# Kernel optimization log

Measured on AMD Instinct MI355X. Metric: run time of the kernel, lower is better.

Reference implementation:

```python
import jax, jax.numpy as jnp
import numpy as np

N = 50000      # nodes
E = 800000     # edges (before self loops)
IN = 61        # input node features
H = 256        # hidden
HEADS = 8
C = H // HEADS # per-head channels = 32
L = 4          # GAT layers
EPS = 1e-5


def setup_inputs() -> dict:
    key = jax.random.key(0)
    ks = jax.random.split(key, 10)
    s = 0.05
    return {
        "x": jax.random.normal(ks[0], (N, IN), jnp.float32),
        "edge_index": jax.random.randint(ks[1], (2, E), 0, N),
        "in_W": jax.random.normal(ks[2], (IN, H), jnp.float32) * s,
        "in_b": jnp.zeros((H,), jnp.float32),
        "in_gamma": jnp.ones((H,), jnp.float32),
        "in_beta": jnp.zeros((H,), jnp.float32),
        "Ws": jax.random.normal(ks[3], (L, H, H), jnp.float32) * s,
        "att_src": jax.random.normal(ks[4], (L, HEADS, C), jnp.float32) * s,
        "att_dst": jax.random.normal(ks[5], (L, HEADS, C), jnp.float32) * s,
        "conv_b": jnp.zeros((L, H), jnp.float32),
        "bn_gamma": jnp.ones((L, H), jnp.float32),
        "bn_beta": jnp.zeros((L, H), jnp.float32),
        "mean_W": jax.random.normal(ks[6], (H, 1), jnp.float32) * s,
        "mean_b": jnp.zeros((1,), jnp.float32),
        "lv_W": jax.random.normal(ks[7], (H, 1), jnp.float32) * s,
        "lv_b": jnp.zeros((1,), jnp.float32),
    }


def _bn(h, gamma, beta):
    # training-mode BatchNorm1d: batch stats, biased variance
    mu = h.mean(axis=0)
    var = jnp.var(h, axis=0)
    return (h - mu) * jax.lax.rsqrt(var + EPS) * gamma + beta


def _gat_layer(h, src, dst, W, a_src, a_dst, bias):
    # h: [N,H] -> z: [N,HEADS,C]
    z = (h @ W).reshape(N, HEADS, C)
    e_src = jnp.einsum('nhc,hc->nh', z, a_src)  # [N,HEADS]
    e_dst = jnp.einsum('nhc,hc->nh', z, a_dst)
    e = jax.nn.leaky_relu(e_src[src] + e_dst[dst], 0.2)  # [Etot,HEADS]
    # segment softmax over destination neighborhoods
    emax = jax.ops.segment_max(e, dst, num_segments=N)
    p = jnp.exp(e - emax[dst])
    denom = jax.ops.segment_sum(p, dst, num_segments=N)
    alpha = p / denom[dst]
    # weighted scatter-aggregate of per-edge messages
    out = jax.ops.segment_sum(z[src] * alpha[:, :, None], dst, num_segments=N)
    return out.reshape(N, H) + bias


def reference(x, edge_index, in_W, in_b, in_gamma, in_beta, Ws, att_src,
              att_dst, conv_b, bn_gamma, bn_beta, mean_W, mean_b, lv_W, lv_b):
    loops = jnp.arange(N, dtype=edge_index.dtype)
    src = jnp.concatenate([edge_index[0], loops])  # add_self_loops=True
    dst = jnp.concatenate([edge_index[1], loops])
    # input projection: Linear -> BN -> ReLU (dropout off, deterministic)
    h = jax.nn.relu(_bn(x @ in_W + in_b, in_gamma, in_beta))
    for i in range(L):
        res = h
        h = _gat_layer(h, src, dst, Ws[i], att_src[i], att_dst[i], conv_b[i])
        h = jax.nn.relu(_bn(h, bn_gamma[i], bn_beta[i])) + res
    mean = (h @ mean_W + mean_b)[:, 0]
    log_var = jnp.clip((h @ lv_W + lv_b)[:, 0], -10.0, 10.0)
    return (mean, log_var)
```

## Files before the change

### kernel.cpp

```cpp
#include <hip/hip_runtime.h>
#include <hip/hip_fp16.h>

#define NN 50000
#define EE 800000
#define ETOT 850000
#define KIN 61
#define HH 256
#define NH 8
#define CC 32
#define LL 4
#define SCAN_NBLK 49

typedef __attribute__((ext_vector_type(8))) short bf16x8;
typedef __attribute__((ext_vector_type(4))) float f32x4;

__device__ __forceinline__ unsigned short f2b(float f) {
    unsigned u = __builtin_bit_cast(unsigned, f);
    u += 0x7fffu + ((u >> 16) & 1u);
    return (unsigned short)(u >> 16);
}
__device__ __forceinline__ float b2f(unsigned short h) {
    unsigned u = ((unsigned)h) << 16;
    return __builtin_bit_cast(float, u);
}
__device__ __forceinline__ unsigned short f2h(float f) {
    __half h = __float2half(f);
    return __builtin_bit_cast(unsigned short, h);
}

__device__ __forceinline__ void gload16(const void* g, void* l) {
    __builtin_amdgcn_global_load_lds(
        (const __attribute__((address_space(1))) void*)g,
        (__attribute__((address_space(3))) void*)l, 16, 0, 0);
}


__global__ __launch_bounds__(256) void edge_hist(const int* __restrict__ ei,
                                                 int* __restrict__ counts) {
    int e = blockIdx.x * 256 + threadIdx.x;
    if (e >= ETOT) return;
    int d = (e < EE) ? ei[EE + e] : (e - EE);
    atomicAdd(&counts[d], 1);
}

__global__ __launch_bounds__(256) void scan1(const int* __restrict__ counts,
                                             int* __restrict__ tmp,
                                             int* __restrict__ bsums) {
    __shared__ int lds[256];
    int b = blockIdx.x, t = threadIdx.x;
    int base = b * 1024 + t * 4;
    int v0 = 0, v1 = 0, v2 = 0, v3 = 0;
    if (base + 0 < NN) v0 = counts[base + 0];
    if (base + 1 < NN) v1 = counts[base + 1];
    if (base + 2 < NN) v2 = counts[base + 2];
    if (base + 3 < NN) v3 = counts[base + 3];
    int s = v0 + v1 + v2 + v3;
    lds[t] = s;
    __syncthreads();
    for (int off = 1; off < 256; off <<= 1) {
        int x = (t >= off) ? lds[t - off] : 0;
        __syncthreads();
        lds[t] += x;
        __syncthreads();
    }
    int run = lds[t] - s;
    if (t == 255) bsums[b] = lds[255];
    run += v0; if (base + 0 < NN) tmp[base + 0] = run;
    run += v1; if (base + 1 < NN) tmp[base + 1] = run;
    run += v2; if (base + 2 < NN) tmp[base + 2] = run;
    run += v3; if (base + 3 < NN) tmp[base + 3] = run;
}

__global__ void scan2(int* __restrict__ bsums) {
    if (threadIdx.x == 0) {
        int acc = 0;
        for (int i = 0; i < SCAN_NBLK; ++i) { int t = bsums[i]; bsums[i] = acc; acc += t; }
    }
}

__global__ __launch_bounds__(256) void scan3(const int* __restrict__ tmp,
                                             const int* __restrict__ bsums,
                                             const int* __restrict__ counts,
                                             int* __restrict__ rowptr,
                                             int* __restrict__ cursor) {
    int i = blockIdx.x * 256 + threadIdx.x;
    if (i >= NN) return;
    int incl = tmp[i] + bsums[i >> 10];
    rowptr[i + 1] = incl;
    cursor[i] = incl - counts[i];
    if (i == 0) rowptr[0] = 0;
}

__global__ __launch_bounds__(256) void edge_scatter(const int* __restrict__ ei,
                                                    int* __restrict__ cursor,
                                                    int* __restrict__ ssrc) {
    int e = blockIdx.x * 256 + threadIdx.x;
    if (e >= ETOT) return;
    int s, d;
    if (e < EE) { s = ei[e]; d = ei[EE + e]; } else { s = d = e - EE; }
    int pos = atomicAdd(&cursor[d], 1);
    ssrc[pos] = s;
}

__global__ __launch_bounds__(256) void sort_rows(const int* __restrict__ rowptr,
                                                 int* __restrict__ ssrc) {
    int wid = (blockIdx.x * 256 + threadIdx.x) >> 6;
    int lane = threadIdx.x & 63;
    if (wid >= NN) return;
    int beg = rowptr[wid], end = rowptr[wid + 1];
    int L = end - beg;
    if (L > 64) return;
    int v = (lane < L) ? ssrc[beg + lane] : 0x7fffffff;
#pragma unroll
    for (int k = 2; k <= 64; k <<= 1) {
#pragma unroll
        for (int j = k >> 1; j > 0; j >>= 1) {
            int partner = __shfl_xor(v, j);
            bool up = ((lane & k) == 0);
            bool keepMin = (up == ((lane & j) == 0));
            int mn = min(v, partner), mx = max(v, partner);
            v = keepMin ? mn : mx;
        }
    }
    if (lane < L) ssrc[beg + lane] = v;
}


__global__ __launch_bounds__(256) void prep_wt(const float* __restrict__ Ws,
                                               unsigned short* __restrict__ WT) {
    int t = blockIdx.x * 256 + threadIdx.x;
    if (t >= LL * HH * HH) return;
    int l = t >> 16, rem = t & 65535;
    int n = rem >> 8, k = rem & 255;
    WT[t] = f2b(Ws[l * 65536 + k * HH + n]);
}

__global__ __launch_bounds__(256) void prep_inwt(const float* __restrict__ in_W,
                                                 unsigned short* __restrict__ WT) {
    int t = blockIdx.x * 256 + threadIdx.x;
    if (t >= HH * 64) return;
    int n = t >> 6, k = t & 63;
    WT[t] = (k < KIN) ? f2b(in_W[k * HH + n]) : 0;
}

__global__ __launch_bounds__(256) void prep_x(const float* __restrict__ x,
                                              unsigned short* __restrict__ xb) {
    int t = blockIdx.x * 256 + threadIdx.x;
    if (t >= NN * 64) return;
    int n = t >> 6, c = t & 63;
    xb[t] = (c < KIN) ? f2b(x[n * KIN + c]) : 0;
}

template<int MODE>
__global__ __launch_bounds__(512) void gemm_mfma(const unsigned short* __restrict__ Asrc,
                                                 const unsigned short* __restrict__ Bt,
                                                 unsigned short* __restrict__ C,
                                                 const float* __restrict__ asl,
                                                 const float* __restrict__ adl,
                                                 float* __restrict__ esrcT,
                                                 float* __restrict__ edstT,
                                                 const float* __restrict__ sums,
                                                 const float* __restrict__ gamma,
                                                 const float* __restrict__ beta,
                                                 const unsigned short* __restrict__ res,
                                                 unsigned short* __restrict__ hbNew,
                                                 int M, int K) {
    __shared__ unsigned short As[128 * 64];
    __shared__ unsigned short Bs[256 * 64];
    __shared__ float scaleS[256], shiftS[256];
    int row0 = blockIdx.x * 128;
    int tid = threadIdx.x;
    int w = tid >> 6, l = tid & 63;
    int wm = w >> 2, wn = w & 3;
    int r15 = l & 15, q = l >> 4;

    if constexpr (MODE == 1) {
        if (tid < 256) {
            const float invN = 1.f / NN;
            float mn = sums[tid] * invN;
            float var = fmaxf(sums[256 + tid] * invN - mn * mn, 0.f);
            float rs = rsqrtf(var + 1e-5f);
            float sc = rs * gamma[tid];
            scaleS[tid] = sc;
            shiftS[tid] = beta[tid] - mn * sc;
        }
        __syncthreads();
    }

    f32x4 acc[4][4] = {};

    int crow = l >> 3;
    int cs   = l & 7;

    for (int kt = 0; kt < K; kt += 64) {
        if (kt) __syncthreads();
#pragma unroll
        for (int c = 0; c < 2; ++c) {
            int r = w * 16 + c * 8 + crow;
            int sg = cs ^ (r & 7);
            int ga = row0 + r;
            if constexpr (MODE == 0) {
                if (ga >= M) ga = M - 1;
                gload16(&Asrc[(size_t)ga * K + kt + sg * 8], &As[(w * 16 + c * 8) * 64]);
            } else {
                unsigned short* dst = &As[(w * 16 + c * 8) * 64 + l * 8];
                if (ga < M) {
                    int ch = kt + sg * 8;
                    ushort4 xlo = *(const ushort4*)&Asrc[(size_t)ga * 256 + ch];
                    ushort4 xhi = *(const ushort4*)&Asrc[(size_t)ga * 256 + ch + 4];
                    float4 sc0 = *(const float4*)&scaleS[ch];
                    float4 sc1 = *(const float4*)&scaleS[ch + 4];
                    float4 sh0 = *(const float4*)&shiftS[ch];
                    float4 sh1 = *(const float4*)&shiftS[ch + 4];
                    float f0 = fmaxf(b2f(xlo.x) * sc0.x + sh0.x, 0.f);
                    float f1 = fmaxf(b2f(xlo.y) * sc0.y + sh0.y, 0.f);
                    float f2 = fmaxf(b2f(xlo.z) * sc0.z + sh0.z, 0.f);
                    float f3 = fmaxf(b2f(xlo.w) * sc0.w + sh0.w, 0.f);
                    float f4 = fmaxf(b2f(xhi.x) * sc1.x + sh1.x, 0.f);
                    float f5 = fmaxf(b2f(xhi.y) * sc1.y + sh1.y, 0.f);
                    float f6 = fmaxf(b2f(xhi.z) * sc1.z + sh1.z, 0.f);
                    float f7 = fmaxf(b2f(xhi.w) * sc1.w + sh1.w, 0.f);
                    if (res) {
                        ushort4 rlo = *(const ushort4*)&res[(size_t)ga * 256 + ch];
                        ushort4 rhi = *(const ushort4*)&res[(size_t)ga * 256 + ch + 4];
                        f0 += b2f(rlo.x); f1 += b2f(rlo.y); f2 += b2f(rlo.z); f3 += b2f(rlo.w);
                        f4 += b2f(rhi.x); f5 += b2f(rhi.y); f6 += b2f(rhi.z); f7 += b2f(rhi.w);
                    }
                    ushort4 olo, ohi;
                    olo.x = f2b(f0); olo.y = f2b(f1); olo.z = f2b(f2); olo.w = f2b(f3);
                    ohi.x = f2b(f4); ohi.y = f2b(f5); ohi.z = f2b(f6); ohi.w = f2b(f7);
                    *(ushort4*)dst = olo;
                    *(ushort4*)(dst + 4) = ohi;
                    *(ushort4*)&hbNew[(size_t)ga * 256 + ch] = olo;
                    *(ushort4*)&hbNew[(size_t)ga * 256 + ch + 4] = ohi;
                } else {
                    ushort4 zz = {0, 0, 0, 0};
                    *(ushort4*)dst = zz;
                    *(ushort4*)(dst + 4) = zz;
                }
            }
        }
#pragma unroll
        for (int c = 0; c < 4; ++c) {
            int r = w * 32 + c * 8 + crow;
            int sg = cs ^ (r & 7);
            gload16(&Bt[(size_t)r * K + kt + sg * 8], &Bs[(w * 32 + c * 8) * 64]);
        }
        __syncthreads();
#pragma unroll
        for (int kk = 0; kk < 2; ++kk) {
            bf16x8 aF[4], bF[4];
#pragma unroll
            for (int i = 0; i < 4; ++i) {
                int ar = wm * 64 + i * 16 + r15;
                aF[i] = *(bf16x8*)&As[ar * 64 + ((kk * 4 + q) ^ (ar & 7)) * 8];
                int br = wn * 64 + i * 16 + r15;
                bF[i] = *(bf16x8*)&Bs[br * 64 + ((kk * 4 + q) ^ (br & 7)) * 8];
            }
#pragma unroll
            for (int i = 0; i < 4; ++i)
#pragma unroll
                for (int j = 0; j < 4; ++j)
                    acc[i][j] = __builtin_amdgcn_mfma_f32_16x16x32_bf16(aF[i], bF[j], acc[i][j], 0, 0, 0);
        }
    }

#pragma unroll
    for (int i = 0; i < 4; ++i)
#pragma unroll
        for (int j = 0; j < 4; ++j) {
            int nc = wn * 64 + j * 16 + r15;
#pragma unroll
            for (int r = 0; r < 4; ++r) {
                int gr = row0 + wm * 64 + i * 16 + q * 4 + r;
                if (gr < M) {
                    if (MODE == 1)
                        C[(size_t)(nc >> 5) * NN * CC + (size_t)gr * CC + (nc & 31)] = f2h(acc[i][j][r]);
                    else
                        C[(size_t)gr * HH + nc] = f2b(acc[i][j][r]);
                }
            }
        }

    if constexpr (MODE == 1) {
        int hdbase = wn * 2;
        float as_[4], ad_[4];
#pragma unroll
        for (int j = 0; j < 4; ++j) {
            int idx = (hdbase + (j >> 1)) * CC + (j & 1) * 16 + r15;
            as_[j] = asl[idx];
            ad_[j] = adl[idx];
        }
#pragma unroll
        for (int h = 0; h < 2; ++h) {
#pragma unroll
            for (int i = 0; i < 4; ++i) {
                float pes[4], ped[4];
#pragma unroll
                for (int r = 0; r < 4; ++r) {
                    float v0 = __half2float(__float2half(acc[i][2 * h][r]));
                    float v1 = __half2float(__float2half(acc[i][2 * h + 1][r]));
                    pes[r] = v0 * as_[2 * h] + v1 * as_[2 * h + 1];
                    ped[r] = v0 * ad_[2 * h] + v1 * ad_[2 * h + 1];
                }
#pragma unroll
                for (int off = 1; off <= 8; off <<= 1) {
#pragma unroll
                    for (int r = 0; r < 4; ++r) {
                        pes[r] += __shfl_xor(pes[r], off);
                        ped[r] += __shfl_xor(ped[r], off);
                    }
                }
                int hd = hdbase + h;
                if (r15 < 8) {
                    int r = r15 & 3;
                    int gr = row0 + wm * 64 + i * 16 + q * 4 + r;
                    if (gr < M) {
                        if (r15 < 4) esrcT[(size_t)hd * NN + gr] = pes[r];
                        else         edstT[(size_t)hd * NN + gr] = ped[r];
                    }
                }
            }
        }
    }
}

#define MAXEB 2048
__global__ __launch_bounds__(256) void aggregate(const int* __restrict__ rowptr,
                                                 const int* __restrict__ ssrc,
                                                 const float* __restrict__ esrcT,
                                                 const float* __restrict__ edstT,
                                                 const unsigned short* __restrict__ zT,
                                                 unsigned short* __restrict__ outb,
                                                 float* __restrict__ sums) {
    __shared__ int   s_lds[MAXEB];
    __shared__ float p_lds[MAXEB];
    __shared__ int   rp_lds[33];
    __shared__ float ed_lds[32];
    __shared__ float ws1[4][8][4], ws2[4][8][4];
    int bid = blockIdx.x;
    int hd = bid & 7;
    int n0 = (bid >> 3) * 32;
    int tid = threadIdx.x;
    const float* esp = esrcT + (size_t)hd * NN;
    const unsigned short* zp = zT + (size_t)hd * NN * CC;

    if (tid <= 32) {
        int idx = n0 + tid;
        rp_lds[tid] = rowptr[idx > NN ? NN : idx];
    }
    if (tid < 32) {
        int nn = n0 + tid;
        ed_lds[tid] = (nn < NN) ? edstT[(size_t)hd * NN + nn] : 0.f;
    }
    __syncthreads();
    int beg0 = rp_lds[0];
    int total = rp_lds[32] - beg0;
    bool staged = (total <= MAXEB);
    if (staged) {
        for (int j = tid; j < total; j += 256) {
            int s = ssrc[beg0 + j];
            int jj = beg0 + j;
            int lo = 0, hi = 32;
#pragma unroll
            for (int st = 0; st < 5; ++st) {
                int mid = (lo + hi) >> 1;
                bool le = (rp_lds[mid] <= jj);
                lo = le ? mid : lo;
                hi = le ? hi : mid;
            }
            float e = esp[s] + ed_lds[lo];
            e = (e > 0.f) ? e : 0.2f * e;
            s_lds[j] = s;
            p_lds[j] = __expf(e);
        }
    }
    __syncthreads();

    int lane = tid & 63;
    int wv = tid >> 6;
    int g = lane >> 3;
    int nl = wv * 8 + g;
    int n = n0 + nl;
    int col = (lane & 7) * 4;
    bool act = n < NN;
    int jbeg = rp_lds[nl] - beg0;
    int jend = rp_lds[nl + 1] - beg0;

    float d0 = 0.f, d1 = 0.f, d2 = 0.f, d3 = 0.f;
    __half2 zero2 = __float2half2_rn(0.f);
    __half2 c0l = zero2, c0h = zero2, c1l = zero2, c1h = zero2;
    __half2 c2l = zero2, c2h = zero2, c3l = zero2, c3h = zero2;
    int j = jbeg;
    if (staged) {
        for (; j + 3 < jend; j += 4) {
            int s0 = s_lds[j], s1 = s_lds[j + 1], s2 = s_lds[j + 2], s3 = s_lds[j + 3];
            float p0 = p_lds[j], p1 = p_lds[j + 1], p2 = p_lds[j + 2], p3 = p_lds[j + 3];
            uint2 z0 = *(const uint2*)&zp[(size_t)(s0 * CC + col)];
            uint2 z1 = *(const uint2*)&zp[(size_t)(s1 * CC + col)];
            uint2 z2 = *(const uint2*)&zp[(size_t)(s2 * CC + col)];
            uint2 z3 = *(const uint2*)&zp[(size_t)(s3 * CC + col)];
            __half2 ph0 = __float2half2_rn(p0 * 0.0625f);
            __half2 ph1 = __float2half2_rn(p1 * 0.0625f);
            __half2 ph2 = __float2half2_rn(p2 * 0.0625f);
            __half2 ph3 = __float2half2_rn(p3 * 0.0625f);
            d0 += p0; d1 += p1; d2 += p2; d3 += p3;
            c0l = __hfma2(ph0, __builtin_bit_cast(__half2, z0.x), c0l);
            c0h = __hfma2(ph0, __builtin_bit_cast(__half2, z0.y), c0h);
            c1l = __hfma2(ph1, __builtin_bit_cast(__half2, z1.x), c1l);
            c1h = __hfma2(ph1, __builtin_bit_cast(__half2, z1.y), c1h);
            c2l = __hfma2(ph2, __builtin_bit_cast(__half2, z2.x), c2l);
            c2h = __hfma2(ph2, __builtin_bit_cast(__half2, z2.y), c2h);
            c3l = __hfma2(ph3, __builtin_bit_cast(__half2, z3.x), c3l);
            c3h = __hfma2(ph3, __builtin_bit_cast(__half2, z3.y), c3h);
        }
        for (; j < jend; ++j) {
            int s0 = s_lds[j];
            float p0 = p_lds[j];
            uint2 z0 = *(const uint2*)&zp[(size_t)(s0 * CC + col)];
            __half2 ph0 = __float2half2_rn(p0 * 0.0625f);
            d0 += p0;
            c0l = __hfma2(ph0, __builtin_bit_cast(__half2, z0.x), c0l);
            c0h = __hfma2(ph0, __builtin_bit_cast(__half2, z0.y), c0h);
        }
    } else {
        float ed = act ? ed_lds[nl] : 0.f;
        for (; j < jend; ++j) {
            int s0 = ssrc[beg0 + j];
            float es0 = esp[s0];
            uint2 z0 = *(const uint2*)&zp[(size_t)(s0 * CC + col)];
            float e0 = es0 + ed; e0 = (e0 > 0.f) ? e0 : 0.2f * e0;
            float p0 = __expf(e0);
            __half2 ph0 = __float2half2_rn(p0 * 0.0625f);
            d0 += p0;
            c0l = __hfma2(ph0, __builtin_bit_cast(__half2, z0.x), c0l);
            c0h = __hfma2(ph0, __builtin_bit_cast(__half2, z0.y), c0h);
        }
    }
    float v0 = 0.f, v1 = 0.f, v2 = 0.f, v3 = 0.f;
    if (act) {
        float den = (d0 + d1) + (d2 + d3);
        float inv = 16.f / den;
        float2 f0l = __half22float2(c0l), f1l = __half22float2(c1l);
        float2 f2l = __half22float2(c2l), f3l = __half22float2(c3l);
        float2 f0h = __half22float2(c0h), f1h = __half22float2(c1h);
        float2 f2h_ = __half22float2(c2h), f3h = __half22float2(c3h);
        ushort4 o;
        o.x = f2b(((f0l.x + f1l.x) + (f2l.x + f3l.x)) * inv);
        o.y = f2b(((f0l.y + f1l.y) + (f2l.y + f3l.y)) * inv);
        o.z = f2b(((f0h.x + f1h.x) + (f2h_.x + f3h.x)) * inv);
        o.w = f2b(((f0h.y + f1h.y) + (f2h_.y + f3h.y)) * inv);
        *(ushort4*)&outb[(size_t)n * HH + hd * CC + col] = o;
        v0 = b2f(o.x); v1 = b2f(o.y); v2 = b2f(o.z); v3 = b2f(o.w);
    }
    float q0 = v0 * v0, q1 = v1 * v1, q2 = v2 * v2, q3 = v3 * v3;
#pragma unroll
    for (int off = 8; off <= 32; off <<= 1) {
        v0 += __shfl_xor(v0, off); v1 += __shfl_xor(v1, off);
        v2 += __shfl_xor(v2, off); v3 += __shfl_xor(v3, off);
        q0 += __shfl_xor(q0, off); q1 += __shfl_xor(q1, off);
        q2 += __shfl_xor(q2, off); q3 += __shfl_xor(q3, off);
    }
    if (g == 0) {
        int slot = lane & 7;
        ws1[wv][slot][0] = v0; ws1[wv][slot][1] = v1;
        ws1[wv][slot][2] = v2; ws1[wv][slot][3] = v3;
        ws2[wv][slot][0] = q0; ws2[wv][slot][1] = q1;
        ws2[wv][slot][2] = q2; ws2[wv][slot][3] = q3;
    }
    __syncthreads();
    if (tid < 32) {
        int slot = tid & 7, k = tid >> 3;
        float s1v = ws1[0][slot][k] + ws1[1][slot][k] + ws1[2][slot][k] + ws1[3][slot][k];
        float s2v = ws2[0][slot][k] + ws2[1][slot][k] + ws2[2][slot][k] + ws2[3][slot][k];
        int ch = hd * CC + slot * 4 + k;
        atomicAdd(&sums[ch], s1v);
        atomicAdd(&sums[HH + ch], s2v);
    }
}

__global__ __launch_bounds__(256) void col_stats(const unsigned short* __restrict__ X,
                                                 float* __restrict__ sums) {
    int c = threadIdx.x;
    int rows_per_block = (NN + gridDim.x - 1) / gridDim.x;
    int r0 = blockIdx.x * rows_per_block;
    int r1 = min(NN, r0 + rows_per_block);
    float s = 0.f, q = 0.f;
    for (int r = r0; r < r1; ++r) {
        float v = b2f(X[(size_t)r * HH + c]);
        s += v; q += v * v;
    }
    atomicAdd(&sums[c], s);
    atomicAdd(&sums[HH + c], q);
}

__global__ __launch_bounds__(256) void bn_out(const unsigned short* __restrict__ X,
                                              const float* __restrict__ sums,
                                              const float* __restrict__ gamma,
                                              const float* __restrict__ beta,
                                              const unsigned short* __restrict__ res,
                                              const float* __restrict__ mW,
                                              const float* __restrict__ mb,
                                              const float* __restrict__ lW,
                                              const float* __restrict__ lb,
                                              float* __restrict__ out) {
    int i = blockIdx.x * 256 + threadIdx.x;
    int row = i >> 6;
    int lane = threadIdx.x & 63;
    int c4 = (i & 63) * 4;
    const float invN = 1.f / NN;
    ushort4 u = *(const ushort4*)(X + (size_t)i * 4);
    float v0 = b2f(u.x), v1 = b2f(u.y), v2 = b2f(u.z), v3 = b2f(u.w);
    float4 s1 = *(const float4*)&sums[c4];
    float4 s2 = *(const float4*)&sums[HH + c4];
    float4 gm = *(const float4*)&gamma[c4];
    float4 bt = *(const float4*)&beta[c4];
    float mn0 = s1.x * invN, mn1 = s1.y * invN, mn2 = s1.z * invN, mn3 = s1.w * invN;
    float rs0 = rsqrtf(fmaxf(s2.x * invN - mn0 * mn0, 0.f) + 1e-5f);
    float rs1 = rsqrtf(fmaxf(s2.y * invN - mn1 * mn1, 0.f) + 1e-5f);
    float rs2 = rsqrtf(fmaxf(s2.z * invN - mn2 * mn2, 0.f) + 1e-5f);
    float rs3 = rsqrtf(fmaxf(s2.w * invN - mn3 * mn3, 0.f) + 1e-5f);
    float r0 = fmaxf((v0 - mn0) * rs0 * gm.x + bt.x, 0.f);
    float r1 = fmaxf((v1 - mn1) * rs1 * gm.y + bt.y, 0.f);
    float r2 = fmaxf((v2 - mn2) * rs2 * gm.z + bt.z, 0.f);
    float r3 = fmaxf((v3 - mn3) * rs3 * gm.w + bt.w, 0.f);
    ushort4 rv = *(const ushort4*)(res + (size_t)i * 4);
    r0 += b2f(rv.x); r1 += b2f(rv.y); r2 += b2f(rv.z); r3 += b2f(rv.w);
    float4 wv = *(const float4*)&mW[c4];
    float4 lv = *(const float4*)&lW[c4];
    float sm = r0 * wv.x + r1 * wv.y + r2 * wv.z + r3 * wv.w;
    float sl = r0 * lv.x + r1 * lv.y + r2 * lv.z + r3 * lv.w;
    for (int off = 32; off > 0; off >>= 1) {
        sm += __shfl_down(sm, off);
        sl += __shfl_down(sl, off);
    }
    if (lane == 0) {
        out[row] = sm + mb[0];
        float l2 = sl + lb[0];
        out[NN + row] = fminf(10.f, fmaxf(-10.f, l2));
    }
}

extern "C" void kernel_launch(void* const* d_in, const int* in_sizes, int n_in,
                              void* d_out, int out_size, void* d_ws, size_t ws_size,
                              hipStream_t stream) {
    const float* x        = (const float*)d_in[0];
    const int*   ei       = (const int*)d_in[1];
    const float* in_W     = (const float*)d_in[2];
    const float* in_gamma = (const float*)d_in[4];
    const float* in_beta  = (const float*)d_in[5];
    const float* Ws       = (const float*)d_in[6];
    const float* att_src  = (const float*)d_in[7];
    const float* att_dst  = (const float*)d_in[8];
    const float* bn_gamma = (const float*)d_in[10];
    const float* bn_beta  = (const float*)d_in[11];
    const float* mean_W   = (const float*)d_in[12];
    const float* mean_b   = (const float*)d_in[13];
    const float* lv_W     = (const float*)d_in[14];
    const float* lv_b     = (const float*)d_in[15];
    float* out = (float*)d_out;

    char* p = (char*)d_ws;
    unsigned short* z    = (unsigned short*)p; p += (size_t)NN * HH * 2;
    unsigned short* hb   = (unsigned short*)p; p += (size_t)NN * HH * 2;
    unsigned short* aggb = (unsigned short*)p; p += (size_t)NN * HH * 2;
    float* esrcT = (float*)p;                  p += (size_t)NN * NH * 4;
    float* edstT = (float*)p;                  p += (size_t)NN * NH * 4;
    float* sums = (float*)p;                   p += 512 * 4;
    unsigned short* WT   = (unsigned short*)p; p += (size_t)LL * HH * HH * 2;
    unsigned short* inWT = (unsigned short*)p; p += (size_t)HH * 64 * 2;
    int* counts = (int*)p;                     p += (size_t)NN * 4;
    int* rowptr = (int*)p;                     p += (size_t)(NN + 1) * 4;
    int* cursor = (int*)p;                     p += (size_t)NN * 4;
    int* ssrc   = (int*)p;                     p += (size_t)ETOT * 4;
    int* bsums  = (int*)p;                     p += 64 * 4;
    unsigned short* xb = aggb;

    hipMemsetAsync(counts, 0, NN * sizeof(int), stream);
    edge_hist<<<(ETOT + 255) / 256, 256, 0, stream>>>(ei, counts);
    scan1<<<SCAN_NBLK, 256, 0, stream>>>(counts, cursor, bsums);
    scan2<<<1, 64, 0, stream>>>(bsums);
    scan3<<<(NN + 255) / 256, 256, 0, stream>>>(cursor, bsums, counts, rowptr, cursor);
    edge_scatter<<<(ETOT + 255) / 256, 256, 0, stream>>>(ei, cursor, ssrc);
    sort_rows<<<(NN * 64 + 255) / 256, 256, 0, stream>>>(rowptr, ssrc);

    prep_wt<<<(LL * HH * HH + 255) / 256, 256, 0, stream>>>(Ws, WT);
    prep_inwt<<<(HH * 64 + 255) / 256, 256, 0, stream>>>(in_W, inWT);
    prep_x<<<(NN * 64 + 255) / 256, 256, 0, stream>>>(x, xb);

    gemm_mfma<0><<<(NN + 127) / 128, 512, 0, stream>>>(xb, inWT, hb, nullptr, nullptr,
                                                       nullptr, nullptr, nullptr,
                                                       nullptr, nullptr, nullptr,
                                                       nullptr, NN, 64);
    hipMemsetAsync(sums, 0, 512 * sizeof(float), stream);
    col_stats<<<1024, 256, 0, stream>>>(hb, sums);

    for (int l = 0; l < LL; ++l) {
        const unsigned short* WTl = WT + (size_t)l * HH * HH;
        const float* asl = att_src + (size_t)l * NH * CC;
        const float* adl = att_dst + (size_t)l * NH * CC;
        const unsigned short* bnX = (l == 0) ? hb : aggb;
        const unsigned short* resp = (l == 0) ? nullptr : hb;
        const float* gm = (l == 0) ? in_gamma : bn_gamma + (size_t)(l - 1) * HH;
        const float* bt = (l == 0) ? in_beta  : bn_beta  + (size_t)(l - 1) * HH;

        gemm_mfma<1><<<(NN + 127) / 128, 512, 0, stream>>>(bnX, WTl, z, asl, adl,
                                                           esrcT, edstT, sums, gm, bt,
                                                           resp, hb, NN, HH);
        hipMemsetAsync(sums, 0, 512 * sizeof(float), stream);
        aggregate<<<((NN + 31) / 32) * 8, 256, 0, stream>>>(rowptr, ssrc, esrcT, edstT,
                                                            z, aggb, sums);
    }

    bn_out<<<(NN * 64) / 256, 256, 0, stream>>>(aggb, sums, bn_gamma + 3 * HH,
                                                bn_beta + 3 * HH, hb,
                                                mean_W, mean_b, lv_W, lv_b, out);
}
```

Baseline: 656.4 us.

## Fold attention vectors into weights and fuse input BN stats into GEMM

Precomputes W·a_src and W·a_dst as 16 extra bf16 weight columns, so the per-node attention logits come from extra MFMAs inside the layer GEMM. This replaces the fp16 rounding, multiply and cross-lane shuffle reduction in the epilogue. It also removes the separate col_stats kernel by accumulating column sums and squares with atomics in the input-projection GEMM epilogue. The trade-offs are extra shared memory and MFMA work on one wave column, a change in the rounding path of the attention logits (bf16 weights instead of fp16 z values), and many atomic adds on the sums buffer.

Result: faster. 607.7 us (-7.4%).

```diff
diff --git a/kernel.cpp b/kernel.cpp
--- a/kernel.cpp
+++ b/kernel.cpp
@@ -135,6 +135,23 @@
     WT[t] = f2b(Ws[l * 65536 + k * HH + n]);
 }
 
+__global__ __launch_bounds__(256) void prep_wa(const float* __restrict__ Ws,
+                                               const float* __restrict__ att_src,
+                                               const float* __restrict__ att_dst,
+                                               unsigned short* __restrict__ WaT) {
+    int t = blockIdx.x * 256 + threadIdx.x;
+    if (t >= LL * 16 * 256) return;
+    int l = t >> 12, rem = t & 4095;
+    int oc = rem >> 8, k = rem & 255;
+    int hd = oc & 7;
+    const float* a = ((oc < 8) ? att_src : att_dst) + ((size_t)l * NH + hd) * CC;
+    const float* Wl = Ws + (size_t)l * 65536 + (size_t)k * HH + hd * CC;
+    float s = 0.f;
+#pragma unroll
+    for (int c = 0; c < CC; ++c) s += Wl[c] * a[c];
+    WaT[t] = f2b(s);
+}
+
 __global__ __launch_bounds__(256) void prep_inwt(const float* __restrict__ in_W,
                                                  unsigned short* __restrict__ WT) {
     int t = blockIdx.x * 256 + threadIdx.x;
@@ -154,19 +171,18 @@
 template<int MODE>
 __global__ __launch_bounds__(512) void gemm_mfma(const unsigned short* __restrict__ Asrc,
                                                  const unsigned short* __restrict__ Bt,
+                                                 const unsigned short* __restrict__ WaTl,
                                                  unsigned short* __restrict__ C,
-                                                 const float* __restrict__ asl,
-                                                 const float* __restrict__ adl,
                                                  float* __restrict__ esrcT,
                                                  float* __restrict__ edstT,
-                                                 const float* __restrict__ sums,
+                                                 float* __restrict__ sums,
                                                  const float* __restrict__ gamma,
                                                  const float* __restrict__ beta,
                                                  const unsigned short* __restrict__ res,
                                                  unsigned short* __restrict__ hbNew,
                                                  int M, int K) {
     __shared__ unsigned short As[128 * 64];
-    __shared__ unsigned short Bs[256 * 64];
+    __shared__ unsigned short Bs[272 * 64];
     __shared__ float scaleS[256], shiftS[256];
     int row0 = blockIdx.x * 128;
     int tid = threadIdx.x;
@@ -188,6 +204,7 @@
     }
 
     f32x4 acc[4][4] = {};
+    f32x4 accX[4] = {};
 
     int crow = l >> 3;
     int cs   = l & 7;
@@ -246,6 +263,13 @@
             int sg = cs ^ (r & 7);
             gload16(&Bt[(size_t)r * K + kt + sg * 8], &Bs[(w * 32 + c * 8) * 64]);
         }
+        if constexpr (MODE == 1) {
+            if (w < 2) {
+                int rr = w * 8 + crow;
+                int sg = cs ^ (crow & 7);
+                gload16(&WaTl[(size_t)rr * K + kt + sg * 8], &Bs[(256 + w * 8) * 64]);
+            }
+        }
         __syncthreads();
 #pragma unroll
         for (int kk = 0; kk < 2; ++kk) {
@@ -262,6 +286,15 @@
 #pragma unroll
                 for (int j = 0; j < 4; ++j)
                     acc[i][j] = __builtin_amdgcn_mfma_f32_16x16x32_bf16(aF[i], bF[j], acc[i][j], 0, 0, 0);
+            if constexpr (MODE == 1) {
+                if (wn == 0) {
+                    int br = 256 + r15;
+                    bf16x8 bX = *(bf16x8*)&Bs[br * 64 + ((kk * 4 + q) ^ (br & 7)) * 8];
+#pragma unroll
+                    for (int i = 0; i < 4; ++i)
+                        accX[i] = __builtin_amdgcn_mfma_f32_16x16x32_bf16(aF[i], bX, accX[i], 0, 0, 0);
+                }
+            }
         }
     }
 
@@ -283,43 +316,37 @@
         }
 
     if constexpr (MODE == 1) {
-        int hdbase = wn * 2;
-        float as_[4], ad_[4];
+        if (wn == 0) {
+            int hd = r15 & 7;
+            float* dstp = (r15 < 8) ? esrcT : edstT;
+#pragma unroll
+            for (int i = 0; i < 4; ++i)
+#pragma unroll
+                for (int r = 0; r < 4; ++r) {
+                    int gr = row0 + wm * 64 + i * 16 + q * 4 + r;
+                    if (gr < M) dstp[(size_t)hd * NN + gr] = accX[i][r];
+                }
+        }
+    } else {
 #pragma unroll
         for (int j = 0; j < 4; ++j) {
-            int idx = (hdbase + (j >> 1)) * CC + (j & 1) * 16 + r15;
-            as_[j] = asl[idx];
-            ad_[j] = adl[idx];
-        }
-#pragma unroll
-        for (int h = 0; h < 2; ++h) {
-#pragma unroll
-            for (int i = 0; i < 4; ++i) {
-                float pes[4], ped[4];
+            float v = 0.f, qq = 0.f;
+#pragma unroll
+            for (int i = 0; i < 4; ++i)
 #pragma unroll
                 for (int r = 0; r < 4; ++r) {
-                    float v0 = __half2float(__float2half(acc[i][2 * h][r]));
-                    float v1 = __half2float(__float2half(acc[i][2 * h + 1][r]));
-                    pes[r] = v0 * as_[2 * h] + v1 * as_[2 * h + 1];
-                    ped[r] = v0 * ad_[2 * h] + v1 * ad_[2 * h + 1];
-                }
-#pragma unroll
-                for (int off = 1; off <= 8; off <<= 1) {
-#pragma unroll
-                    for (int r = 0; r < 4; ++r) {
-                        pes[r] += __shfl_xor(pes[r], off);
-                        ped[r] += __shfl_xor(ped[r], off);
+                    int gr = row0 + wm * 64 + i * 16 + q * 4 + r;
+                    if (gr < M) {
+                        float f = b2f(f2b(acc[i][j][r]));
+                        v += f; qq += f * f;
                     }
                 }
-                int hd = hdbase + h;
-                if (r15 < 8) {
-                    int r = r15 & 3;
-                    int gr = row0 + wm * 64 + i * 16 + q * 4 + r;
-                    if (gr < M) {
-                        if (r15 < 4) esrcT[(size_t)hd * NN + gr] = pes[r];
-                        else         edstT[(size_t)hd * NN + gr] = ped[r];
-                    }
-                }
+            v += __shfl_xor(v, 16); qq += __shfl_xor(qq, 16);
+            v += __shfl_xor(v, 32); qq += __shfl_xor(qq, 32);
+            if (q == 0) {
+                int nc = wn * 64 + j * 16 + r15;
+                atomicAdd(&sums[nc], v);
+                atomicAdd(&sums[HH + nc], qq);
             }
         }
     }
@@ -477,21 +504,6 @@
         atomicAdd(&sums[ch], s1v);
         atomicAdd(&sums[HH + ch], s2v);
     }
-}
-
-__global__ __launch_bounds__(256) void col_stats(const unsigned short* __restrict__ X,
-                                                 float* __restrict__ sums) {
-    int c = threadIdx.x;
-    int rows_per_block = (NN + gridDim.x - 1) / gridDim.x;
-    int r0 = blockIdx.x * rows_per_block;
-    int r1 = min(NN, r0 + rows_per_block);
-    float s = 0.f, q = 0.f;
-    for (int r = r0; r < r1; ++r) {
-        float v = b2f(X[(size_t)r * HH + c]);
-        s += v; q += v * v;
-    }
-    atomicAdd(&sums[c], s);
-    atomicAdd(&sums[HH + c], q);
 }
 
 __global__ __launch_bounds__(256) void bn_out(const unsigned short* __restrict__ X,
@@ -568,6 +580,7 @@
     float* edstT = (float*)p;                  p += (size_t)NN * NH * 4;
     float* sums = (float*)p;                   p += 512 * 4;
     unsigned short* WT   = (unsigned short*)p; p += (size_t)LL * HH * HH * 2;
+    unsigned short* WaT  = (unsigned short*)p; p += (size_t)LL * 16 * HH * 2;
     unsigned short* inWT = (unsigned short*)p; p += (size_t)HH * 64 * 2;
     int* counts = (int*)p;                     p += (size_t)NN * 4;
     int* rowptr = (int*)p;                     p += (size_t)(NN + 1) * 4;
@@ -585,26 +598,25 @@
     sort_rows<<<(NN * 64 + 255) / 256, 256, 0, stream>>>(rowptr, ssrc);
 
     prep_wt<<<(LL * HH * HH + 255) / 256, 256, 0, stream>>>(Ws, WT);
+    prep_wa<<<(LL * 16 * HH + 255) / 256, 256, 0, stream>>>(Ws, att_src, att_dst, WaT);
     prep_inwt<<<(HH * 64 + 255) / 256, 256, 0, stream>>>(in_W, inWT);
     prep_x<<<(NN * 64 + 255) / 256, 256, 0, stream>>>(x, xb);
 
-    gemm_mfma<0><<<(NN + 127) / 128, 512, 0, stream>>>(xb, inWT, hb, nullptr, nullptr,
-                                                       nullptr, nullptr, nullptr,
+    hipMemsetAsync(sums, 0, 512 * sizeof(float), stream);
+    gemm_mfma<0><<<(NN + 127) / 128, 512, 0, stream>>>(xb, inWT, nullptr, hb,
+                                                       nullptr, nullptr, sums,
                                                        nullptr, nullptr, nullptr,
                                                        nullptr, NN, 64);
-    hipMemsetAsync(sums, 0, 512 * sizeof(float), stream);
-    col_stats<<<1024, 256, 0, stream>>>(hb, sums);
 
     for (int l = 0; l < LL; ++l) {
         const unsigned short* WTl = WT + (size_t)l * HH * HH;
-        const float* asl = att_src + (size_t)l * NH * CC;
-        const float* adl = att_dst + (size_t)l * NH * CC;
+        const unsigned short* WaTl = WaT + (size_t)l * 16 * HH;
         const unsigned short* bnX = (l == 0) ? hb : aggb;
         const unsigned short* resp = (l == 0) ? nullptr : hb;
         const float* gm = (l == 0) ? in_gamma : bn_gamma + (size_t)(l - 1) * HH;
         const float* bt = (l == 0) ? in_beta  : bn_beta  + (size_t)(l - 1) * HH;
 
-        gemm_mfma<1><<<(NN + 127) / 128, 512, 0, stream>>>(bnX, WTl, z, asl, adl,
+        gemm_mfma<1><<<(NN + 127) / 128, 512, 0, stream>>>(bnX, WTl, WaTl, z,
                                                            esrcT, edstT, sums, gm, bt,
                                                            resp, hb, NN, HH);
         hipMemsetAsync(sums, 0, 512 * sizeof(float), stream);
```
